# Optimization experiments

Measured on AMD Instinct MI355X. Metric: run time of the kernel, lower is better.

Reference implementation:

```python
import jax, jax.numpy as jnp
import numpy as np

# dims: Q queries, K hops (topk), N relation groups, M padded nodes/group
Q, K, N, M = 64, 2, 32, 64
E, D, R, S = 256, 1024, 200, 8192  # embs_size, model_size, n_rel, seq positions


def setup_inputs() -> dict:
    key = jax.random.key(0)
    ks = jax.random.split(key, 10)
    hidden_states = jax.random.normal(ks[0], (S, D), jnp.float32)
    nodes = jax.random.normal(ks[1], (Q, K, N, M, E), jnp.float32)
    # ragged groups: zero-pad beyond a random valid length (mirrors F.pad + stack)
    lengths = jax.random.randint(ks[2], (Q, K, N), 1, M + 1)
    valid = jnp.arange(M)[None, None, None, :] < lengths[..., None]
    nodes = nodes * valid[..., None]
    prob_idx = jax.random.randint(ks[3], (Q, K, N), 0, R)
    gnn_idx = jnp.arange(Q, dtype=jnp.int32)          # gnn_mask positions
    rel_idx = jnp.arange(Q, dtype=jnp.int32) + Q      # rel_mask positions (disjoint)
    sc = lambda fan: float(1.0 / np.sqrt(fan))
    u = lambda k, shp, fan: jax.random.uniform(k, shp, jnp.float32, -sc(fan), sc(fan))
    Wc = u(ks[4], (D, R), D); bc = jnp.zeros((R,), jnp.float32)
    Wq = u(ks[5], (D, D), D); bq = jnp.zeros((D,), jnp.float32)
    Wn = u(ks[6], (E, D), E); bn = jnp.zeros((D,), jnp.float32)
    Wg = u(ks[7], (E, D), E); bg = jnp.zeros((D,), jnp.float32)
    return {"hidden_states": hidden_states, "nodes": nodes, "prob_idx": prob_idx,
            "gnn_idx": gnn_idx, "rel_idx": rel_idx,
            "Wc": Wc, "bc": bc, "Wq": Wq, "bq": bq,
            "Wn": Wn, "bn": bn, "Wg": Wg, "bg": bg}


def reference(hidden_states, nodes, prob_idx, gnn_idx, rel_idx,
              Wc, bc, Wq, bq, Wn, bn, Wg, bg):
    Qn, Kn, Nn, Mn, En = nodes.shape
    # classification_head: Linear + Softmax over relations
    rel_prob = jax.nn.softmax(hidden_states[rel_idx] @ Wc + bc, axis=1)  # [Q,R]
    # gather per-group relation probabilities (extract_values_from_tensor)
    probs = jnp.take_along_axis(rel_prob, prob_idx.reshape(Qn, Kn * Nn), axis=1)
    probs = probs.reshape(Qn, Kn, Nn)                                     # [Q,K,N]
    # mask from first feature of padded node embeddings (as in calculate_scores)
    mask = nodes[..., 0] != 0                                             # [Q,K,N,M]
    # query_reprj and nodes_reprj (Linear + Tanh)
    gq = jnp.tanh(hidden_states[gnn_idx] @ Wq + bq)                       # [Q,D]
    gn = jnp.tanh(jnp.einsum('qknme,ed->qknmd', nodes, Wn) + bn)          # [Q,K,N,M,D]
    dots = jnp.einsum('qknmd,qd->qknm', gn, gq)                           # [Q,K,N,M]
    attn = jax.nn.softmax(dots, axis=3)            # softmax over nodes within group
    logits = attn * probs[..., None] / 0.1         # scale by group prob / temperature
    # global softmax over all (group, node) slots per (query, hop)
    wa = jax.nn.softmax(logits.reshape(Qn, Kn, Nn * Mn), axis=-1)
    wa = wa.reshape(Qn, Kn, Nn, Mn)
    wa = jnp.where(mask, wa, 0.0)
    # weighted mean over the flattened N*M slots, then mean over topk hops
    mean_emb = jnp.mean(nodes * wa[..., None], axis=(2, 3))               # [Q,K,E]
    pooled = mean_emb.mean(axis=1)                                        # [Q,E]
    out = jnp.tanh(pooled @ Wg + bg)                                      # gnn_reprj
    return hidden_states.at[gnn_idx].add(out)
```

## Files before the change

### kernel.cpp

```cpp
#include <hip/hip_runtime.h>
#include <hip/hip_bf16.h>
#include <math.h>

#define QDIM 64
#define KDIM 2
#define NDIM 32
#define MDIM 64
#define EDIM 256
#define DDIM 1024
#define RDIM 200
#define SDIM 8192
#define GCOUNT (QDIM * KDIM * NDIM)

#define GLOBAL_AS __attribute__((address_space(1)))
#define LDS_AS __attribute__((address_space(3)))

typedef short short8_t __attribute__((ext_vector_type(8)));
typedef float f32x4 __attribute__((ext_vector_type(4)));

__device__ __forceinline__ float tanh_c(float x) {
    float e = __expf(2.0f * x);
    return 1.0f - 2.0f * __builtin_amdgcn_rcpf(1.0f + e);
}

__device__ __forceinline__ uint32_t f2bf(float f) {
    uint32_t u = __float_as_uint(f);
    return (u + 0x7fffu + ((u >> 16) & 1u)) >> 16;
}
__device__ __forceinline__ float bf2f(unsigned short h) {
    return __uint_as_float(((uint32_t)h) << 16);
}

__global__ __launch_bounds__(256) void prologue_kernel(
    const float* __restrict__ hs, float* __restrict__ out,
    const float* __restrict__ Wn, short* __restrict__ wnpk,
    const int* __restrict__ gnn_idx, const float* __restrict__ Wq,
    const float* __restrict__ bq, float* __restrict__ gqo,
    const int* __restrict__ rel_idx, const float* __restrict__ Wc,
    const float* __restrict__ bc, float* __restrict__ rel_prob,
    const float* __restrict__ nodes, int* __restrict__ nvarr) {
    const int b = blockIdx.x, t = threadIdx.x;
    __shared__ float row[DDIM];
    __shared__ float arr[256];

    if (b < 2048) {
        const float4* src = (const float4*)hs;
        float4* dst = (float4*)out;
        int i = b * 256 + t;
#pragma unroll
        for (int r = 0; r < 4; ++r) dst[i + r * 524288] = src[i + r * 524288];
    } else if (b < 2176) {
        int tid = (b - 2048) * 256 + t;
        int lane = tid & 63, ks = (tid >> 6) & 7, ntg = tid >> 9;
        int low = lane & 15, hi = lane >> 4;
        short8_t o;
#pragma unroll
        for (int j = 0; j < 8; ++j) {
            int k = ks * 32 + hi * 8 + j;
            int d = ntg * 16 + low;
            o[j] = (short)f2bf(Wn[(size_t)k * DDIM + d]);
        }
        *(short8_t*)(wnpk + (size_t)tid * 8) = o;
    } else if (b < 2432) {
        int bb = b - 2176;
        int q = bb >> 2, seg = bb & 3;
        const float* src = hs + (size_t)gnn_idx[q] * DDIM;
        for (int i = t; i < DDIM; i += 256) row[i] = src[i];
        __syncthreads();
        int d = seg * 256 + t;
        float a = bq[d];
#pragma unroll 8
        for (int k = 0; k < DDIM; ++k) a += row[k] * Wq[(size_t)k * DDIM + d];
        gqo[(size_t)q * DDIM + d] = tanh_c(a);
    } else if (b < 2496) {
        int q = b - 2432;
        const float* src = hs + (size_t)rel_idx[q] * DDIM;
        for (int i = t; i < DDIM; i += 256) row[i] = src[i];
        __syncthreads();
        float lg = -INFINITY;
        if (t < RDIM) {
            float a = bc[t];
            for (int k = 0; k < DDIM; ++k) a += row[k] * Wc[(size_t)k * RDIM + t];
            lg = a;
        }
        arr[t] = lg;
        __syncthreads();
        for (int s = 128; s > 0; s >>= 1) {
            if (t < s) arr[t] = fmaxf(arr[t], arr[t + s]);
            __syncthreads();
        }
        float mx = arr[0];
        __syncthreads();
        float ex = (t < RDIM) ? __expf(lg - mx) : 0.0f;
        arr[t] = ex;
        __syncthreads();
        for (int s = 128; s > 0; s >>= 1) {
            if (t < s) arr[t] += arr[t + s];
            __syncthreads();
        }
        float sm = arr[0];
        if (t < RDIM) rel_prob[q * RDIM + t] = ex / sm;
    } else {
        int g = (b - 2496) * 4 + (t >> 6);
        int lane = t & 63;
        float f0 = nodes[(size_t)g * (MDIM * EDIM) + (size_t)lane * EDIM];
        unsigned long long mk = __ballot(f0 != 0.0f);
        if (lane == 0) nvarr[g] = __popcll(mk);
    }
}

__global__ __launch_bounds__(64) void pack_jobs(const int* __restrict__ nvarr,
                                                const float* __restrict__ bn,
                                                const float* __restrict__ gq,
                                                int4* __restrict__ glist4,
                                                float* __restrict__ cqarr) {
    int q = blockIdx.x, t = threadIdx.x;
    __shared__ int lists[4][64];
    __shared__ int cnt[4];
    float cp = 0.f;
#pragma unroll
    for (int i = 0; i < 16; ++i) {
        int d = i * 64 + t;
        cp += tanh_c(bn[d]) * gq[(size_t)q * DDIM + d];
    }
#pragma unroll
    for (int off = 32; off > 0; off >>= 1) cp += __shfl_xor(cp, off);
    if (t == 0) cqarr[q] = cp;

    if (t < 4) cnt[t] = 0;
    __syncthreads();
    int g = q * 64 + t;
    int nv = nvarr[g];
    int mt = (nv + 15) >> 4;
    if (mt < 1) mt = 1;
    if (mt > 4) mt = 4;
    int pos = atomicAdd(&cnt[mt - 1], 1);
    lists[mt - 1][pos] = g;
    __syncthreads();
    if (t == 0) {
        int c1 = cnt[0], c2 = cnt[1], c3 = cnt[2], c4 = cnt[3];
        int i1 = 0, i2 = 0, i3 = 0, i4 = 0, j = 0;
        int4* outp = glist4 + q * 64;
        const int D = GCOUNT;
        while (i4 < c4) outp[j++] = make_int4(lists[3][i4++] | (0 << 20), D, D, D);
        while (i3 < c3) {
            int g1 = (i1 < c1) ? lists[0][i1++] : D;
            outp[j++] = make_int4(lists[2][i3++] | (1 << 20), g1, D, D);
        }
        while (i2 + 1 < c2) {
            int a = lists[1][i2++], b2 = lists[1][i2++];
            outp[j++] = make_int4(a | (2 << 20), b2, D, D);
        }
        if (i2 < c2) {
            int a = lists[1][i2++];
            int b2 = (i1 < c1) ? lists[0][i1++] : D;
            int c = (i1 < c1) ? lists[0][i1++] : D;
            outp[j++] = make_int4(a | (3 << 20), b2, c, D);
        }
        while (i1 < c1) {
            int a = lists[0][i1++];
            int b2 = (i1 < c1) ? lists[0][i1++] : D;
            int c = (i1 < c1) ? lists[0][i1++] : D;
            int d2 = (i1 < c1) ? lists[0][i1++] : D;
            outp[j++] = make_int4(a | (4 << 20), b2, c, d2);
        }
        while (j < 64) outp[j++] = make_int4(-1, -1, -1, -1);
    }
}

__global__ __launch_bounds__(256, 3) void phase1_mfma(
    const float* __restrict__ nodes, const short* __restrict__ wnpk,
    const float* __restrict__ bn, const float* __restrict__ gq,
    const float* __restrict__ rel_prob, const int* __restrict__ prob_idx,
    const int4* __restrict__ glist4, const float* __restrict__ cqarr,
    float* __restrict__ gvec, float* __restrict__ gden, float* __restrict__ gmx) {
    __shared__ alignas(16) char lds[34304];
    float2* pairs = (float2*)(lds + 16384);
    float(*vecu)[EDIM] = (float(*)[EDIM])(lds + 24576);
    float* dots_s = (float*)(lds + 32768);
    float* lv_s = dots_s + 128;
    float* mk_s = lv_s + 128;

    const int tid = threadIdx.x;
    const int w = tid >> 6, lane = tid & 63;
    const int low = lane & 15, hi = lane >> 4;

    const int4 jb0 = glist4[2 * blockIdx.x];
    const int4 jb1 = glist4[2 * blockIdx.x + 1];
    if (jb0.x < 0 && jb1.x < 0) return;
    const int4 jb = (w < 2) ? jb0 : jb1;
    const bool live = jb.x >= 0;
    const int q = ((jb0.x >= 0 ? jb0.x : jb1.x) & 0xFFFF) >> 6;
    const float cqv = cqarr[q];

    const unsigned tabs[5] = {0x30201000u, 0x01201000u, 0x11011000u, 0x02011000u,
                              0x03020100u};
    const int gA[4] = {jb.x & 0xFFFF, jb.y, jb.z, jb.w};
    const unsigned tb = live ? tabs[(jb.x >> 20) & 7] : 0;

    int usrc[2] = {GCOUNT, GCOUNT};
    short8_t af[2][8];
    if (live) {
        char* ldsw = lds + w * 8192;
#pragma unroll
        for (int u2 = 0; u2 < 2; ++u2) {
            int u = (w & 1) * 2 + u2;
            int byte_ = (tb >> (u * 8)) & 0xFF;
            int slot = byte_ & 0xF, tile = byte_ >> 4;
            int gs = gA[slot];
            usrc[u2] = gs;
            int lg = (gs >= GCOUNT) ? 0 : gs;
            const float4* src =
                (const float4*)(nodes + ((size_t)lg * MDIM + tile * 16) * EDIM);
#pragma unroll
            for (int i = 0; i < 16; ++i) {
                int idx4 = i * 64 + lane;
                float4 v = src[idx4];
                int r = idx4 >> 6, c4 = idx4 & 63;
                int off = (r * 512 + c4 * 8) ^ ((r & 7) << 4);
                uint32_t w0 = f2bf(v.x) | (f2bf(v.y) << 16);
                uint32_t w1 = f2bf(v.z) | (f2bf(v.w) << 16);
                *(uint2*)(ldsw + off) = make_uint2(w0, w1);
            }
            asm volatile("s_waitcnt lgkmcnt(0)" ::: "memory");
#pragma unroll
            for (int ks = 0; ks < 8; ++ks) {
                int off = (low * 512 + ks * 64 + hi * 16) ^ ((low & 7) << 4);
                af[u2][ks] = *(const short8_t*)(ldsw + off);
            }
            asm volatile("s_waitcnt lgkmcnt(0)" ::: "memory");
        }
    }
    __syncthreads();

    {
        const float* gqrow = gq + (size_t)q * DDIM;
#pragma unroll
        for (int i = 0; i < 4; ++i) {
            int d = tid + i * 256;
            pairs[d] = make_float2(bn[d], gqrow[d]);
        }
    }
#define STAGE_B(NT, BUF)                                                            \
    {                                                                               \
        const short* sb_ = wnpk + (size_t)(NT)*4096;                                \
        _Pragma("unroll") for (int c_ = 0; c_ < 2; ++c_) {                          \
            int seg_ = (w * 2 + c_) * 512;                              \
            __builtin_amdgcn_global_load_lds(                                       \
                (const GLOBAL_AS void*)(sb_ + seg_ + lane * 8),                     \
                (LDS_AS void*)(lds + (BUF)*8192 + seg_ * 2), 16, 0, 0);             \
        }                                                                           \
    }
    STAGE_B(0, 0);
    asm volatile("s_waitcnt vmcnt(0)" ::: "memory");
    __syncthreads();

    float dacc[2][4] = {};
    for (int it = 0; it < 64; ++it) {
        const int cur = it & 1;
        if (it < 63) STAGE_B(it + 1, cur ^ 1);
        if (live) {
            const short8_t* bp = (const short8_t*)(lds + cur * 8192) + lane;
            short8_t bf[8];
#pragma unroll
            for (int ks = 0; ks < 8; ++ks) bf[ks] = bp[ks * 64];
            float2 pv = pairs[it * 16 + low];
            f32x4 a0 = {0.f, 0.f, 0.f, 0.f}, a1 = a0;
#pragma unroll
            for (int ks = 0; ks < 8; ++ks) {
                a0 = __builtin_amdgcn_mfma_f32_16x16x32_bf16(af[0][ks], bf[ks], a0, 0, 0, 0);
                a1 = __builtin_amdgcn_mfma_f32_16x16x32_bf16(af[1][ks], bf[ks], a1, 0, 0, 0);
            }
            float bnv = pv.x, gqv = pv.y;
#pragma unroll
            for (int jj = 0; jj < 4; ++jj) {
                dacc[0][jj] += tanh_c(a0[jj] + bnv) * gqv;
                dacc[1][jj] += tanh_c(a1[jj] + bnv) * gqv;
            }
        }
        asm volatile("s_waitcnt vmcnt(0)" ::: "memory");
        __syncthreads();
    }

    if (live) {
#pragma unroll
        for (int u2 = 0; u2 < 2; ++u2)
#pragma unroll
            for (int jj = 0; jj < 4; ++jj) {
                float v = dacc[u2][jj];
                v += __shfl_xor(v, 1);
                v += __shfl_xor(v, 2);
                v += __shfl_xor(v, 4);
                v += __shfl_xor(v, 8);
                dacc[u2][jj] = v;
            }
        if (low == 0) {
#pragma unroll
            for (int u2 = 0; u2 < 2; ++u2)
#pragma unroll
                for (int jj = 0; jj < 4; ++jj)
                    dots_s[(w * 2 + u2) * 16 + hi * 4 + jj] = dacc[u2][jj];
        }
        if (hi == 0) {
#pragma unroll
            for (int u2 = 0; u2 < 2; ++u2) {
                unsigned short s0 = (unsigned short)af[u2][0][0];
                mk_s[(w * 2 + u2) * 16 + low] = ((s0 & 0x7fffu) != 0) ? 1.0f : 0.0f;
            }
        }
    }
    __syncthreads();

    const int NGT[5] = {1, 2, 2, 3, 4};
    const int U0T[5][4] = {{0, 0, 0, 0}, {0, 3, 0, 0}, {0, 2, 0, 0},
                           {0, 2, 3, 0}, {0, 1, 2, 3}};
    const int NUT[5][4] = {{4, 0, 0, 0}, {3, 1, 0, 0}, {2, 2, 0, 0},
                           {2, 1, 1, 0}, {1, 1, 1, 1}};
    const int ng0 = (jb0.x >= 0) ? NGT[(jb0.x >> 20) & 7] : 0;
    const int ng1 = (jb1.x >= 0) ? NGT[(jb1.x >> 20) & 7] : 0;
    const int ngtot = ng0 + ng1;

    for (int gi = w; gi < ngtot; gi += 4) {
        int jx = (gi < ng0) ? 0 : 1;
        int4 J = jx ? jb1 : jb0;
        int li = jx ? gi - ng0 : gi;
        int shp = (J.x >> 20) & 7;
        int U0 = U0T[shp][li] + jx * 4;
        int NU = NUT[shp][li];
        int gg = (li == 0) ? (J.x & 0xFFFF) : (li == 1) ? J.y : (li == 2) ? J.z : J.w;
        if (gg >= GCOUNT) continue;
        int NS = NU * 16, TL = 64 - NS;
        float dv = (lane < NS) ? dots_s[U0 * 16 + lane] : -INFINITY;
        float mx = dv;
#pragma unroll
        for (int o = 32; o > 0; o >>= 1) mx = fmaxf(mx, __shfl_xor(mx, o));
        if (TL > 0) mx = fmaxf(mx, cqv);
        float ex = (lane < NS) ? __expf(dv - mx) : 0.f;
        float sm = ex;
#pragma unroll
        for (int o = 32; o > 0; o >>= 1) sm += __shfl_xor(sm, o);
        float ext = __expf(cqv - mx);
        if (TL > 0) sm += (float)TL * ext;
        float pr = rel_prob[(size_t)q * RDIM + prob_idx[gg]];
        float p10 = pr * 10.0f / sm;
        float l2 = ex * p10;
        float lgvt = ext * p10;
        float gm = (lane < NS) ? l2 : -INFINITY;
#pragma unroll
        for (int o = 32; o > 0; o >>= 1) gm = fmaxf(gm, __shfl_xor(gm, o));
        if (TL > 0) gm = fmaxf(gm, lgvt);
        float el = (lane < NS) ? __expf(l2 - gm) : 0.f;
        float den = el;
#pragma unroll
        for (int o = 32; o > 0; o >>= 1) den += __shfl_xor(den, o);
        if (TL > 0) den += (float)TL * __expf(lgvt - gm);
        if (lane < NS) lv_s[U0 * 16 + lane] = el * mk_s[U0 * 16 + lane];
        if (lane == 0) {
            gden[gg] = den;
            gmx[gg] = gm;
        }
    }
    __syncthreads();

    if (live) {
#pragma unroll
        for (int u2 = 0; u2 < 2; ++u2) {
            if (usrc[u2] >= GCOUNT) continue;
            int ug = w * 2 + u2;
            float lvm = lv_s[ug * 16 + low];
#pragma unroll
            for (int ks = 0; ks < 8; ++ks) {
                float acj[8];
#pragma unroll
                for (int j = 0; j < 8; ++j)
                    acj[j] = bf2f((unsigned short)af[u2][ks][j]) * lvm;
#pragma unroll
                for (int j = 0; j < 8; ++j) {
                    float a = acj[j];
                    a += __shfl_xor(a, 1);
                    a += __shfl_xor(a, 2);
                    a += __shfl_xor(a, 4);
                    a += __shfl_xor(a, 8);
                    acj[j] = a;
                }
                if (low == 0) {
#pragma unroll
                    for (int j = 0; j < 8; ++j) vecu[ug][ks * 32 + hi * 8 + j] = acj[j];
                }
            }
        }
    }
    __syncthreads();

    for (int gi = w; gi < ngtot; gi += 4) {
        int jx = (gi < ng0) ? 0 : 1;
        int4 J = jx ? jb1 : jb0;
        int li = jx ? gi - ng0 : gi;
        int shp = (J.x >> 20) & 7;
        int U0 = U0T[shp][li] + jx * 4;
        int NU = NUT[shp][li];
        int gg = (li == 0) ? (J.x & 0xFFFF) : (li == 1) ? J.y : (li == 2) ? J.z : J.w;
        if (gg >= GCOUNT) continue;
#pragma unroll 4
        for (int c = 0; c < 4; ++c) {
            int e = c * 64 + lane;
            float s = 0.f;
            for (int uu = 0; uu < NU; ++uu) s += vecu[U0 + uu][e];
            gvec[(size_t)gg * EDIM + e] = s;
        }
    }
}

__global__ __launch_bounds__(256) void combine_kernel(const float* __restrict__ gvec,
                                                      const float* __restrict__ gden,
                                                      const float* __restrict__ gmx,
                                                      float* __restrict__ memb) {
    int qk = blockIdx.x, t = threadIdx.x;
    __shared__ float sgm[NDIM], sden[NDIM];
    if (t < NDIM) {
        sgm[t] = gmx[qk * NDIM + t];
        sden[t] = gden[qk * NDIM + t];
    }
    __syncthreads();
    float gm = -INFINITY;
    for (int n = 0; n < NDIM; ++n) gm = fmaxf(gm, sgm[n]);
    float gs = 0.f;
    for (int n = 0; n < NDIM; ++n) gs += sden[n] * __expf(sgm[n] - gm);
    float me = 0.f;
    for (int n = 0; n < NDIM; ++n)
        me += gvec[(size_t)(qk * NDIM + n) * EDIM + t] * __expf(sgm[n] - gm);
    memb[(size_t)qk * EDIM + t] = me / (gs * (float)(NDIM * MDIM));
}

__global__ __launch_bounds__(256) void out_kernel(const float* __restrict__ memb,
                                                  const float* __restrict__ Wg,
                                                  const float* __restrict__ bg,
                                                  const int* __restrict__ gnn_idx,
                                                  float* __restrict__ out) {
    int q = blockIdx.x, t = threadIdx.x;
    __shared__ float pooled[EDIM];
    pooled[t] = 0.5f * (memb[(size_t)(q * 2 + 0) * EDIM + t] + memb[(size_t)(q * 2 + 1) * EDIM + t]);
    __syncthreads();
    float4 a = ((const float4*)bg)[t];
    const float4* Wg4 = (const float4*)Wg;
    for (int e = 0; e < EDIM; ++e) {
        float p = pooled[e];
        float4 w = Wg4[(size_t)e * (DDIM / 4) + t];
        a.x += p * w.x; a.y += p * w.y; a.z += p * w.z; a.w += p * w.w;
    }
    float4* op = (float4*)(out + (size_t)gnn_idx[q] * DDIM);
    float4 cur = op[t];
    cur.x += tanh_c(a.x);
    cur.y += tanh_c(a.y);
    cur.z += tanh_c(a.z);
    cur.w += tanh_c(a.w);
    op[t] = cur;
}

extern "C" void kernel_launch(void* const* d_in, const int* in_sizes, int n_in,
                              void* d_out, int out_size, void* d_ws, size_t ws_size,
                              hipStream_t stream) {
    const float* hs = (const float*)d_in[0];
    const float* nodes = (const float*)d_in[1];
    const int* prob_idx = (const int*)d_in[2];
    const int* gnn_idx = (const int*)d_in[3];
    const int* rel_idx = (const int*)d_in[4];
    const float* Wc = (const float*)d_in[5];
    const float* bc = (const float*)d_in[6];
    const float* Wq = (const float*)d_in[7];
    const float* bq = (const float*)d_in[8];
    const float* Wn = (const float*)d_in[9];
    const float* bn = (const float*)d_in[10];
    const float* Wg = (const float*)d_in[11];
    const float* bg = (const float*)d_in[12];
    float* out = (float*)d_out;
    float* ws = (float*)d_ws;

    float* relprob = ws;
    float* gqbuf = ws + 16384;
    float* gvec = gqbuf + 65536;
    float* gdenA = gvec + 1048832;
    float* gmaxA = gdenA + 4352;
    float* membuf = gmaxA + 4352;
    short* wnpk = (short*)(membuf + 32768);
    int* nvarr = (int*)(ws + 1303296);
    int4* glist4 = (int4*)(ws + 1307392);
    float* cqarr = ws + 1323776;

    prologue_kernel<<<3520, 256, 0, stream>>>(hs, out, Wn, wnpk, gnn_idx, Wq, bq,
                                              gqbuf, rel_idx, Wc, bc, relprob,
                                              nodes, nvarr);
    pack_jobs<<<QDIM, 64, 0, stream>>>(nvarr, bn, gqbuf, glist4, cqarr);
    phase1_mfma<<<GCOUNT / 2, 256, 0, stream>>>(nodes, wnpk, bn, gqbuf, relprob,
                                                prob_idx, glist4, cqarr, gvec, gdenA,
                                                gmaxA);
    combine_kernel<<<QDIM * KDIM, 256, 0, stream>>>(gvec, gdenA, gmaxA, membuf);
    out_kernel<<<QDIM, 256, 0, stream>>>(membuf, Wg, bg, gnn_idx, out);
}
```

Before: 269.0 us.

## Triple-buffer Wn staging in phase1 and fuse combine with output projection

The phase1 MFMA loop goes from double to triple buffering of the packed Wn tiles in LDS, prefetching two iterations ahead. It waits with vmcnt(2) and uses one barrier per iteration instead of draining all loads each step. Separately, the combine and out kernels are merged into one per-query kernel, removing a launch and the intermediate memb round trip. LDS use rises by 4 KB per block, which could affect occupancy at the 3-blocks-per-CU launch bound.

New measurement: 268.5 us. Within noise of the previous version (-0.2%).

```diff
diff --git a/kernel.cpp b/kernel.cpp
--- a/kernel.cpp
+++ b/kernel.cpp
@@ -174,10 +174,10 @@
     const float* __restrict__ rel_prob, const int* __restrict__ prob_idx,
     const int4* __restrict__ glist4, const float* __restrict__ cqarr,
     float* __restrict__ gvec, float* __restrict__ gden, float* __restrict__ gmx) {
-    __shared__ alignas(16) char lds[34304];
-    float2* pairs = (float2*)(lds + 16384);
-    float(*vecu)[EDIM] = (float(*)[EDIM])(lds + 24576);
-    float* dots_s = (float*)(lds + 32768);
+    __shared__ alignas(16) char lds[38400];
+    float2* pairs = (float2*)(lds + 24576);
+    float(*vecu)[EDIM] = (float(*)[EDIM])(lds + 32768);
+    float* dots_s = (float*)(lds + 36864);
     float* lv_s = dots_s + 128;
     float* mk_s = lv_s + 128;
 
@@ -252,15 +252,23 @@
         }                                                                           \
     }
     STAGE_B(0, 0);
-    asm volatile("s_waitcnt vmcnt(0)" ::: "memory");
-    __syncthreads();
+    STAGE_B(1, 1);
 
     float dacc[2][4] = {};
+    int rd = 0;
     for (int it = 0; it < 64; ++it) {
-        const int cur = it & 1;
-        if (it < 63) STAGE_B(it + 1, cur ^ 1);
+        if (it < 62) {
+            asm volatile("s_waitcnt vmcnt(2)" ::: "memory");
+        } else {
+            asm volatile("s_waitcnt vmcnt(0)" ::: "memory");
+        }
+        __syncthreads();
+        if (it < 62) {
+            int wr = (rd == 0) ? 2 : rd - 1;
+            STAGE_B(it + 2, wr);
+        }
         if (live) {
-            const short8_t* bp = (const short8_t*)(lds + cur * 8192) + lane;
+            const short8_t* bp = (const short8_t*)(lds + rd * 8192) + lane;
             short8_t bf[8];
 #pragma unroll
             for (int ks = 0; ks < 8; ++ks) bf[ks] = bp[ks * 64];
@@ -278,8 +286,7 @@
                 dacc[1][jj] += tanh_c(a1[jj] + bnv) * gqv;
             }
         }
-        asm volatile("s_waitcnt vmcnt(0)" ::: "memory");
-        __syncthreads();
+        rd = (rd == 2) ? 0 : rd + 1;
     }
 
     if (live) {
@@ -411,35 +418,34 @@
     }
 }
 
-__global__ __launch_bounds__(256) void combine_kernel(const float* __restrict__ gvec,
-                                                      const float* __restrict__ gden,
-                                                      const float* __restrict__ gmx,
-                                                      float* __restrict__ memb) {
-    int qk = blockIdx.x, t = threadIdx.x;
-    __shared__ float sgm[NDIM], sden[NDIM];
-    if (t < NDIM) {
-        sgm[t] = gmx[qk * NDIM + t];
-        sden[t] = gden[qk * NDIM + t];
-    }
-    __syncthreads();
-    float gm = -INFINITY;
-    for (int n = 0; n < NDIM; ++n) gm = fmaxf(gm, sgm[n]);
-    float gs = 0.f;
-    for (int n = 0; n < NDIM; ++n) gs += sden[n] * __expf(sgm[n] - gm);
-    float me = 0.f;
-    for (int n = 0; n < NDIM; ++n)
-        me += gvec[(size_t)(qk * NDIM + n) * EDIM + t] * __expf(sgm[n] - gm);
-    memb[(size_t)qk * EDIM + t] = me / (gs * (float)(NDIM * MDIM));
-}
-
-__global__ __launch_bounds__(256) void out_kernel(const float* __restrict__ memb,
-                                                  const float* __restrict__ Wg,
-                                                  const float* __restrict__ bg,
-                                                  const int* __restrict__ gnn_idx,
-                                                  float* __restrict__ out) {
+__global__ __launch_bounds__(256) void combineout_kernel(
+    const float* __restrict__ gvec, const float* __restrict__ gden,
+    const float* __restrict__ gmx, const float* __restrict__ Wg,
+    const float* __restrict__ bg, const int* __restrict__ gnn_idx,
+    float* __restrict__ out) {
     int q = blockIdx.x, t = threadIdx.x;
+    __shared__ float sgm[2][NDIM], sden[2][NDIM];
     __shared__ float pooled[EDIM];
-    pooled[t] = 0.5f * (memb[(size_t)(q * 2 + 0) * EDIM + t] + memb[(size_t)(q * 2 + 1) * EDIM + t]);
+    if (t < 64) {
+        int k = t >> 5, n = t & 31;
+        sgm[k][n] = gmx[(q * 2 + k) * NDIM + n];
+        sden[k][n] = gden[(q * 2 + k) * NDIM + n];
+    }
+    __syncthreads();
+    float pl = 0.f;
+#pragma unroll
+    for (int k = 0; k < 2; ++k) {
+        float gm = -INFINITY;
+        for (int n = 0; n < NDIM; ++n) gm = fmaxf(gm, sgm[k][n]);
+        float gs = 0.f;
+        for (int n = 0; n < NDIM; ++n) gs += sden[k][n] * __expf(sgm[k][n] - gm);
+        float me = 0.f;
+        for (int n = 0; n < NDIM; ++n)
+            me += gvec[(size_t)((q * 2 + k) * NDIM + n) * EDIM + t] *
+                  __expf(sgm[k][n] - gm);
+        pl += 0.5f * me / (gs * (float)(NDIM * MDIM));
+    }
+    pooled[t] = pl;
     __syncthreads();
     float4 a = ((const float4*)bg)[t];
     const float4* Wg4 = (const float4*)Wg;
@@ -494,6 +500,6 @@
     phase1_mfma<<<GCOUNT / 2, 256, 0, stream>>>(nodes, wnpk, bn, gqbuf, relprob,
                                                 prob_idx, glist4, cqarr, gvec, gdenA,
                                                 gmaxA);
-    combine_kernel<<<QDIM * KDIM, 256, 0, stream>>>(gvec, gdenA, gmaxA, membuf);
-    out_kernel<<<QDIM, 256, 0, stream>>>(membuf, Wg, bg, gnn_idx, out);
-}
+    combineout_kernel<<<QDIM, 256, 0, stream>>>(gvec, gdenA, gmaxA, Wg, bg, gnn_idx,
+                                                out);
+}
```
